# Performance work log

Hardware: AMD Instinct MI355X
Metric: run time of the kernel (lower is better)

Reference implementation:

```python
import jax, jax.numpy as jnp
import numpy as np

B, S, D = 2, 2048, 2048
H, KVH, DH = 16, 4, 128  # n_heads, n_kv_heads, head_dim
N_REP = H // KVH
THETA = 10000.0


def setup_inputs() -> dict:
    key = jax.random.key(0)
    ks = jax.random.split(key, 6)
    x = jax.random.normal(ks[0], (B, S, D), dtype=jnp.float32)
    wq = jax.random.normal(ks[1], (H * DH, D), dtype=jnp.float32) * (D ** -0.5)
    wk = jax.random.normal(ks[2], (KVH * DH, D), dtype=jnp.float32) * (D ** -0.5)
    wv = jax.random.normal(ks[3], (KVH * DH, D), dtype=jnp.float32) * (D ** -0.5)
    wo = jax.random.normal(ks[4], (D, H * DH), dtype=jnp.float32) * (D ** -0.5)
    # RoPE frequencies (complex freqs -> cos/sin), shape [S, DH//2]
    inv_freq = 1.0 / (THETA ** (np.arange(0, DH, 2, dtype=np.float32) / DH))
    angles = np.arange(S, dtype=np.float32)[:, None] * inv_freq[None, :]
    freqs_cos = jnp.asarray(np.cos(angles))
    freqs_sin = jnp.asarray(np.sin(angles))
    # causal additive mask [1,1,S,S]
    neg = jnp.full((S, S), -1e9, dtype=jnp.float32)
    mask = jnp.triu(neg, k=1)[None, None]
    return {"x": x, "freqs_cos": freqs_cos, "freqs_sin": freqs_sin,
            "mask": mask, "wq": wq, "wk": wk, "wv": wv, "wo": wo}


def _rope(t, cos, sin):
    # t: [B,S,h,DH]; cos/sin: [S,DH//2] -> broadcast [1,S,1,DH//2]
    tp = t.reshape(*t.shape[:-1], -1, 2)
    tr, ti = tp[..., 0], tp[..., 1]
    c = cos[None, :, None, :]
    s = sin[None, :, None, :]
    out_r = tr * c - ti * s
    out_i = tr * s + ti * c
    return jnp.stack([out_r, out_i], axis=-1).reshape(t.shape)


def reference(x, freqs_cos, freqs_sin, mask, wq, wk, wv, wo):
    b, s, _ = x.shape
    xq = jnp.einsum('bsd,ed->bse', x, wq).reshape(b, s, H, DH)
    xk = jnp.einsum('bsd,ed->bse', x, wk).reshape(b, s, KVH, DH)
    xv = jnp.einsum('bsd,ed->bse', x, wv).reshape(b, s, KVH, DH)
    xq = _rope(xq, freqs_cos, freqs_sin)
    xk = _rope(xk, freqs_cos, freqs_sin)
    # GQA: repeat kv heads
    xk = jnp.repeat(xk, N_REP, axis=2)
    xv = jnp.repeat(xv, N_REP, axis=2)
    q = xq.transpose(0, 2, 1, 3)  # [B,H,S,DH]
    k = xk.transpose(0, 2, 1, 3)
    v = xv.transpose(0, 2, 1, 3)
    scores = jnp.einsum('bhqd,bhkd->bhqk', q, k) / jnp.sqrt(jnp.float32(DH))
    scores = scores + mask
    attn = jax.nn.softmax(scores.astype(jnp.float32), axis=-1).astype(q.dtype)
    out = jnp.einsum('bhqk,bhkd->bhqd', attn, v)
    out = out.transpose(0, 2, 1, 3).reshape(b, s, H * DH)
    return jnp.einsum('bse,de->bsd', out, wo)
```

## Files before the change

kernel.cpp:

```cpp
#include <hip/hip_runtime.h>

#define Bq   2
#define Sq   2048
#define Dq   2048
#define Hq   16
#define KVHq 4
#define DHq  128

typedef unsigned short u16;
typedef short  bf16x8 __attribute__((ext_vector_type(8)));
typedef float  f32x4  __attribute__((ext_vector_type(4)));
typedef float  f32x16 __attribute__((ext_vector_type(16)));
typedef unsigned short u16x2 __attribute__((ext_vector_type(2)));
typedef unsigned short u16x4 __attribute__((ext_vector_type(4)));
typedef unsigned uu32x4 __attribute__((ext_vector_type(4)));

__device__ __forceinline__ u16 f2bf(float f) {
    unsigned u = __float_as_uint(f);
    u += 0x7fffu + ((u >> 16) & 1u);
    return (u16)(u >> 16);
}
__device__ __forceinline__ float bf2f(u16 s) {
    return __uint_as_float(((unsigned)s) << 16);
}

__device__ __forceinline__ unsigned cvtpk(float a, float b) {
    unsigned r;
    asm("v_cvt_pk_bf16_f32 %0, %1, %2" : "=v"(r) : "v"(a), "v"(b));
    return r;
}
__device__ __forceinline__ void pl32swap(unsigned& a, unsigned& b) {
    asm("v_permlane32_swap_b32 %0, %1" : "+v"(a), "+v"(b));
}
__device__ __forceinline__ bf16x8 mkfrag(unsigned w0, unsigned w1, unsigned w2, unsigned w3) {
    uu32x4 t = {w0, w1, w2, w3};
    return __builtin_bit_cast(bf16x8, t);
}

__global__ void cast_bf16(const float* __restrict__ in, u16* __restrict__ out, int n4) {
    int i = blockIdx.x * 256 + threadIdx.x;
    if (i >= n4) return;
    float4 v = ((const float4*)in)[i];
    u16x4 o;
    o.x = f2bf(v.x); o.y = f2bf(v.y); o.z = f2bf(v.z); o.w = f2bf(v.w);
    ((u16x4*)out)[i] = o;
}

__global__ void cast_weights(const float* __restrict__ wq, const float* __restrict__ wk,
                             const float* __restrict__ wv, const float* __restrict__ wo,
                             u16* __restrict__ wqb, u16* __restrict__ wkvb,
                             u16* __restrict__ wob) {
    int i = blockIdx.x * 256 + threadIdx.x;
    const float4* src; u16x4* dst; int off;
    if (i < 1048576)      { src = (const float4*)wq; dst = (u16x4*)wqb;  off = i; }
    else if (i < 1310720) { src = (const float4*)wk; dst = (u16x4*)wkvb; off = i - 1048576; }
    else if (i < 1572864) { src = (const float4*)wv; dst = (u16x4*)wkvb + 262144; off = i - 1310720; }
    else                  { src = (const float4*)wo; dst = (u16x4*)wob;  off = i - 1572864; }
    float4 v = src[off];
    u16x4 o;
    o.x = f2bf(v.x); o.y = f2bf(v.y); o.z = f2bf(v.z); o.w = f2bf(v.w);
    dst[off] = o;
}

__device__ __forceinline__ void async16(const void* g, void* l) {
    __builtin_amdgcn_global_load_lds(
        (const __attribute__((address_space(1))) unsigned*)g,
        (__attribute__((address_space(3))) unsigned*)l, 16, 0, 0);
}

__device__ __forceinline__ void stc(u16* p, float v)   { *p = f2bf(v); }
__device__ __forceinline__ void stc(float* p, float v) { *p = v; }

template <typename OutT>
__global__ __launch_bounds__(256) void gemm_nt(
    const u16* __restrict__ A, const u16* __restrict__ W, OutT* __restrict__ C,
    int M, int N, int K)
{
    __shared__ __align__(16) u16 lA[128 * 32];
    __shared__ __align__(16) u16 lB[128 * 32];

    const int t    = threadIdx.x;
    const int w    = t >> 6;
    const int lane = t & 63;
    const int lr   = lane & 15;
    const int quad = lane >> 4;
    const int wm   = (w >> 1) * 64, wn = (w & 1) * 64;
    const int bm   = blockIdx.x * 128, bn = blockIdx.y * 128;

    const u16* Ab = A + (size_t)bm * K;
    const u16* Wb = W + (size_t)bn * K;

    const int r0  = t >> 2;
    const int r1  = (256 + t) >> 2;
    const int kc0 = (t & 3) * 8;

    char* la0 = (char*)lA + w * 1024;
    char* la1 = (char*)lA + 4096 + w * 1024;
    char* lb0 = (char*)lB + w * 1024;
    char* lb1 = (char*)lB + 4096 + w * 1024;

    f32x4 acc[4][4] = {};

    for (int kt = 0; kt < K; kt += 32) {
        async16(Ab + (size_t)r0 * K + kt + kc0, la0);
        async16(Ab + (size_t)r1 * K + kt + kc0, la1);
        async16(Wb + (size_t)r0 * K + kt + kc0, lb0);
        async16(Wb + (size_t)r1 * K + kt + kc0, lb1);
        __syncthreads();

        bf16x8 af[4], bfr[4];
#pragma unroll
        for (int i = 0; i < 4; i++)
            af[i] = *(const bf16x8*)&lA[(wm + i * 16 + lr) * 32 + quad * 8];
#pragma unroll
        for (int j = 0; j < 4; j++)
            bfr[j] = *(const bf16x8*)&lB[(wn + j * 16 + lr) * 32 + quad * 8];
#pragma unroll
        for (int i = 0; i < 4; i++)
#pragma unroll
            for (int j = 0; j < 4; j++)
                acc[i][j] = __builtin_amdgcn_mfma_f32_16x16x32_bf16(af[i], bfr[j], acc[i][j], 0, 0, 0);
        __syncthreads();
    }

#pragma unroll
    for (int i = 0; i < 4; i++)
#pragma unroll
        for (int j = 0; j < 4; j++)
#pragma unroll
            for (int r = 0; r < 4; r++) {
                int gm = bm + wm + i * 16 + quad * 4 + r;
                int gn = bn + wn + j * 16 + lr;
                stc(C + (size_t)gm * N + gn, acc[i][j][r]);
            }
}

__global__ void rope_k(u16* __restrict__ T, const float* __restrict__ Cs,
                       const float* __restrict__ Sn, int lognh, int total) {
    int i = blockIdx.x * 256 + threadIdx.x;
    if (i >= total) return;
    int p  = i & 63;
    int sh = i >> 6;
    int s  = (sh >> lognh) & (Sq - 1);
    float c = Cs[s * 64 + p], sn = Sn[s * 64 + p];
    u16x2* ptr = ((u16x2*)T) + i;
    u16x2 v = *ptr;
    float tr = bf2f(v.x), ti = bf2f(v.y);
    u16x2 ov;
    ov.x = f2bf(tr * c - ti * sn);
    ov.y = f2bf(tr * sn + ti * c);
    *ptr = ov;
}

__global__ void rope_kv(u16* __restrict__ KV, const float* __restrict__ Cs,
                        const float* __restrict__ Sn, int total) {
    int i = blockIdx.x * 256 + threadIdx.x;
    if (i >= total) return;
    int p     = i & 63;
    int kvh   = (i >> 6) & 3;
    int token = i >> 8;
    int s     = token & (Sq - 1);
    float c = Cs[s * 64 + p], sn = Sn[s * 64 + p];
    u16x2* ptr = ((u16x2*)KV) + (size_t)token * 512 + kvh * 64 + p;
    u16x2 v = *ptr;
    float tr = bf2f(v.x), ti = bf2f(v.y);
    u16x2 ov;
    ov.x = f2bf(tr * c - ti * sn);
    ov.y = f2bf(tr * sn + ti * c);
    *ptr = ov;
}

__global__ void transpose_v_k(const u16* __restrict__ KV, u16* __restrict__ Vt) {
    __shared__ u16 tile[32][33];
    const int bk = blockIdx.z;
    const int b = bk >> 2, kvh = bk & 3;
    const int s0 = blockIdx.x * 32, d0 = blockIdx.y * 32;
    const int tx = threadIdx.x, ty = threadIdx.y;
    tile[ty][tx] = KV[(size_t)(b * Sq + s0 + ty) * 1024 + 512 + kvh * 128 + d0 + tx];
    __syncthreads();
    Vt[((size_t)bk * DHq + d0 + ty) * Sq + s0 + tx] = tile[tx][ty];
}

#define PSCALE 0.12753102f
#define PBIAS  17.31234049f

__global__ __launch_bounds__(256, 2) void flash_attn_sk2(
    const u16* __restrict__ Q, const u16* __restrict__ KV,
    const u16* __restrict__ Vt, float* __restrict__ Oc, float* __restrict__ Lc)
{
    __shared__ __align__(16) u16 kl[2][4 * 64 * 32];
    __shared__ __align__(16) u16 vl[2][2 * 128 * 32];

    const int bh = blockIdx.x;
    const int b = bh >> 4, h = bh & 15;
    const int kvh = h >> 2;
    const int c = 39 - (int)blockIdx.y;
    int qt, ci, nc;
    if (c < 4)       { qt = c;                    ci = 0;            nc = 1; }
    else if (c < 12) { qt = 4  + ((c - 4) >> 1);  ci = (c - 4) & 1;  nc = 2; }
    else if (c < 24) { qt = 8  + (c - 12) / 3;    ci = (c - 12) % 3; nc = 3; }
    else             { qt = 12 + ((c - 24) >> 2); ci = (c - 24) & 3; nc = 4; }
    const int T  = 2 * (qt + 1);
    const int t0 = (ci * T) / nc, t1 = ((ci + 1) * T) / nc;

    const int tid = threadIdx.x;
    const int w = tid >> 6, lane = tid & 63;
    const int col = lane & 31, hi = lane >> 5;
    const int q0 = qt * 128 + w * 32;
    const int qg = q0 + col;

    const u16* Qp = Q + (size_t)(b * Sq + qg) * (Hq * DHq) + h * DHq + hi * 8;
    bf16x8 qf[8];
#pragma unroll
    for (int ks = 0; ks < 8; ks++) qf[ks] = *(const bf16x8*)(Qp + ks * 16);

    const u16* Kg = KV + (size_t)b * Sq * 1024 + kvh * DHq;
    const u16* Vg = Vt + (size_t)(b * KVHq + kvh) * DHq * Sq;

    const int srow = lane >> 2;
    const int swl  = ((lane & 3) ^ ((lane >> 3) & 3)) * 8;
    const int xsw  = (col >> 1) & 3;

    f32x16 o[4] = {};
    float lsum = 0.f;

    auto STAGE = [&](int kt, int bsel) {
        const int kb = kt * 64;
#pragma unroll
        for (int c4 = 0; c4 < 4; c4++) {
            const u16* g = Kg + (size_t)(kb + w * 16 + srow) * 1024 + c4 * 32 + swl;
            async16(g, (char*)kl[bsel] + (c4 * 2048 + w * 512) * 2 + lane * 16);
        }
#pragma unroll
        for (int c4 = 0; c4 < 4; c4++) {
            const int g2 = c4 & 1, dbase = (c4 >> 1) * 64;
            const u16* g = Vg + (size_t)(dbase + w * 16 + srow) * Sq + kb + g2 * 32 + swl;
            async16(g, (char*)vl[bsel] + (g2 * 4096 + (dbase + w * 16) * 32) * 2 + lane * 16);
        }
    };

    STAGE(t0, 0);
    __syncthreads();

    int cur = 0;
    for (int kt = t0; kt < t1; kt++) {
        if (kt + 1 < t1) STAGE(kt + 1, cur ^ 1);

        const int kb = kt * 64;
        const u16* klc = kl[cur];
        const u16* vlc = vl[cur];

        f32x16 s0 = {}, s1 = {};
        __builtin_amdgcn_s_setprio(1);
#pragma unroll
        for (int ks = 0; ks < 8; ks++) {
            const int ch     = (((ks & 1) * 2 + hi) ^ xsw) * 8;
            const int kkbase = (ks >> 1) * 2048 + ch;
            bf16x8 k0 = *(const bf16x8*)&klc[kkbase + col * 32];
            bf16x8 k1 = *(const bf16x8*)&klc[kkbase + (32 + col) * 32];
            s0 = __builtin_amdgcn_mfma_f32_32x32x16_bf16(k0, qf[ks], s0, 0, 0, 0);
            s1 = __builtin_amdgcn_mfma_f32_32x32x16_bf16(k1, qf[ks], s1, 0, 0, 0);
        }
        __builtin_amdgcn_s_setprio(0);

        float p0a[16], p1a[16];
        float ls = 0.f;
        if (q0 - kb >= 63) {
#pragma unroll
            for (int r = 0; r < 16; r++) {
                float a0 = exp2f(s0[r] * PSCALE - PBIAS);
                float a1 = exp2f(s1[r] * PSCALE - PBIAS);
                ls += a0 + a1;
                p0a[r] = a0; p1a[r] = a1;
            }
        } else {
            const int thr = qg - kb;
#pragma unroll
            for (int r = 0; r < 16; r++) {
                const int kloc = (r & 3) + 8 * (r >> 2) + 4 * hi;
                float a0 = (kloc <= thr)      ? exp2f(s0[r] * PSCALE - PBIAS) : 0.f;
                float a1 = (kloc + 32 <= thr) ? exp2f(s1[r] * PSCALE - PBIAS) : 0.f;
                ls += a0 + a1;
                p0a[r] = a0; p1a[r] = a1;
            }
        }
        lsum += ls;

        __builtin_amdgcn_s_setprio(1);
#define PV_HALF(PARR, KSBASE)                                                      \
        {                                                                          \
            _Pragma("unroll")                                                      \
            for (int k2 = 0; k2 < 2; k2++) {                                       \
                const int bb = k2 * 8;                                             \
                unsigned wa = cvtpk(PARR[bb + 0], PARR[bb + 1]);                   \
                unsigned wb = cvtpk(PARR[bb + 4], PARR[bb + 5]);                   \
                pl32swap(wa, wb);                                                  \
                unsigned wc = cvtpk(PARR[bb + 2], PARR[bb + 3]);                   \
                unsigned wd = cvtpk(PARR[bb + 6], PARR[bb + 7]);                   \
                pl32swap(wc, wd);                                                  \
                bf16x8 pa = mkfrag(wa, wc, wb, wd);                                \
                const int vch   = ((k2 * 2 + hi) ^ xsw) * 8;                       \
                const int vbase = (((KSBASE) >> 1) * 4096) + vch;                  \
                _Pragma("unroll")                                                  \
                for (int n = 0; n < 4; n++) {                                      \
                    bf16x8 vf = *(const bf16x8*)&vlc[vbase + (n * 32 + col) * 32]; \
                    o[n] = __builtin_amdgcn_mfma_f32_32x32x16_bf16(pa, vf, o[n], 0, 0, 0); \
                }                                                                  \
            }                                                                      \
        }
        PV_HALF(p0a, 0)
        PV_HALF(p1a, 2)
#undef PV_HALF
        __builtin_amdgcn_s_setprio(0);

        if (kt + 1 < t1) __syncthreads();
        cur ^= 1;
    }

    float tot = lsum + __shfl_xor(lsum, 32);
    float* Ocb = Oc + (size_t)(bh * 40 + c) * 16384 + (size_t)w * 32 * 128;
    float* Lcb = Lc + (size_t)(bh * 40 + c) * 128 + w * 32;
    if (hi == 0) Lcb[col] = tot;
#pragma unroll
    for (int r = 0; r < 16; r++) {
        const int rloc = (r & 3) + 8 * (r >> 2) + 4 * hi;
#pragma unroll
        for (int n = 0; n < 4; n++)
            Ocb[rloc * 128 + n * 32 + col] = o[n][r];
    }
}

__global__ __launch_bounds__(256) void flash_reduce2(
    const float* __restrict__ Oc, const float* __restrict__ Lc, u16* __restrict__ AO)
{
    const int bh = blockIdx.x;
    const int qt = blockIdx.y;
    const int e  = blockIdx.z * 256 + threadIdx.x;
    const int row = e >> 5, col4 = e & 31;
    int cst, nc;
    if (qt < 4)       { cst = qt;                 nc = 1; }
    else if (qt < 8)  { cst = 4  + 2 * (qt - 4);  nc = 2; }
    else if (qt < 12) { cst = 12 + 3 * (qt - 8);  nc = 3; }
    else              { cst = 24 + 4 * (qt - 12); nc = 4; }
    f32x4 acc = {0.f, 0.f, 0.f, 0.f};
    float l = 0.f;
    for (int i = 0; i < nc; i++) {
        const size_t base = (size_t)(bh * 40 + cst + i);
        acc += ((const f32x4*)(Oc + base * 16384))[e];
        l   += Lc[base * 128 + row];
    }
    const float inv = 1.0f / l;
    const int b = bh >> 4, h = bh & 15;
    u16x4 ov;
    ov.x = f2bf(acc[0] * inv); ov.y = f2bf(acc[1] * inv);
    ov.z = f2bf(acc[2] * inv); ov.w = f2bf(acc[3] * inv);
    u16* dst = AO + (size_t)(b * Sq + qt * 128 + row) * (Hq * DHq) + h * DHq + col4 * 4;
    *(u16x4*)dst = ov;
}

__global__ __launch_bounds__(256) void flash_attn(
    const u16* __restrict__ Q, const u16* __restrict__ KV,
    const u16* __restrict__ Vt, u16* __restrict__ O)
{
    __shared__ __align__(16) u16 plds[4][16 * 72];
    const int bh = blockIdx.x;
    const int b = bh >> 4, h = bh & 15;
    const int kvh = h >> 2;
    const int w = threadIdx.x >> 6, lane = threadIdx.x & 63;
    const int lr = lane & 15, quad = lane >> 4;
    const int yy = gridDim.y - 1 - blockIdx.y;
    const int q0 = yy * 64 + w * 16;

    const u16* Qp = Q + (size_t)(b * Sq + q0 + lr) * (Hq * DHq) + h * DHq + quad * 8;
    bf16x8 qf[4];
#pragma unroll
    for (int kk = 0; kk < 4; kk++) qf[kk] = *(const bf16x8*)(Qp + kk * 32);

    const u16* Kp = KV + (size_t)b * Sq * 1024 + kvh * DHq;
    const u16* Vp = Vt + (size_t)(b * KVHq + kvh) * DHq * Sq;

    f32x4 o[8] = {};
    float lsum[4] = {0.f, 0.f, 0.f, 0.f};

    const int nt = (q0 + 16 + 63) >> 6;
    for (int kt = 0; kt < nt; kt++) {
        const int kb = kt * 64;
        f32x4 s[4] = {};
#pragma unroll
        for (int kk = 0; kk < 4; kk++) {
#pragma unroll
            for (int j = 0; j < 4; j++) {
                bf16x8 kf = *(const bf16x8*)(Kp + (size_t)(kb + j * 16 + lr) * 1024 + kk * 32 + quad * 8);
                s[j] = __builtin_amdgcn_mfma_f32_16x16x32_bf16(qf[kk], kf, s[j], 0, 0, 0);
            }
        }
#pragma unroll
        for (int r = 0; r < 4; r++) {
            const int qg = q0 + quad * 4 + r;
#pragma unroll
            for (int j = 0; j < 4; j++) {
                float v = s[j][r] * PSCALE - PBIAS;
                float p = (kb + j * 16 + lr <= qg) ? exp2f(v) : 0.f;
                lsum[r] += p;
                plds[w][(quad * 4 + r) * 72 + j * 16 + lr] = f2bf(p);
            }
        }
        bf16x8 pa0 = *(const bf16x8*)&plds[w][lr * 72 + quad * 8];
        bf16x8 pa1 = *(const bf16x8*)&plds[w][lr * 72 + 32 + quad * 8];
#pragma unroll
        for (int dt = 0; dt < 8; dt++) {
            bf16x8 v0 = *(const bf16x8*)(Vp + (size_t)(dt * 16 + lr) * Sq + kb + quad * 8);
            bf16x8 v1 = *(const bf16x8*)(Vp + (size_t)(dt * 16 + lr) * Sq + kb + 32 + quad * 8);
            o[dt] = __builtin_amdgcn_mfma_f32_16x16x32_bf16(pa0, v0, o[dt], 0, 0, 0);
            o[dt] = __builtin_amdgcn_mfma_f32_16x16x32_bf16(pa1, v1, o[dt], 0, 0, 0);
        }
    }

    u16* Ob = O + (size_t)(b * Sq) * (Hq * DHq) + h * DHq;
#pragma unroll
    for (int r = 0; r < 4; r++) {
        float t = lsum[r];
        t += __shfl_xor(t, 1);
        t += __shfl_xor(t, 2);
        t += __shfl_xor(t, 4);
        t += __shfl_xor(t, 8);
        const float inv = 1.0f / t;
        const int qg = q0 + quad * 4 + r;
#pragma unroll
        for (int dt = 0; dt < 8; dt++)
            Ob[(size_t)qg * (Hq * DHq) + dt * 16 + lr] = f2bf(o[dt][r] * inv);
    }
}

extern "C" void kernel_launch(void* const* d_in, const int* in_sizes, int n_in,
                              void* d_out, int out_size, void* d_ws, size_t ws_size,
                              hipStream_t stream) {
    const float* x  = (const float*)d_in[0];
    const float* fc = (const float*)d_in[1];
    const float* fs = (const float*)d_in[2];
    const float* wq = (const float*)d_in[4];
    const float* wk = (const float*)d_in[5];
    const float* wv = (const float*)d_in[6];
    const float* wo = (const float*)d_in[7];
    float* out = (float*)d_out;

    char* ws = (char*)d_ws;
    u16* xb   = (u16*)(ws);
    u16* wqb  = (u16*)(ws + 16777216);
    u16* wkvb = (u16*)(ws + 25165824);
    u16* wob  = (u16*)(ws + 29360128);
    u16* Qb   = (u16*)(ws + 37748736);
    u16* KVb  = (u16*)(ws + 54525952);
    u16* Vtb  = (u16*)(ws + 62914560);
    u16* AOb  = (u16*)(ws + 67108864);
    float* Ocb = (float*)(ws + 83886080);
    float* Lcb = (float*)(ws + 167772160);
    const size_t WS_NEED = 168427520;

    cast_bf16<<<8192, 256, 0, stream>>>(x, xb, 2097152);
    cast_weights<<<10240, 256, 0, stream>>>(wq, wk, wv, wo, wqb, wkvb, wob);

    dim3 blk(256);
    gemm_nt<u16><<<dim3(32, 16), blk, 0, stream>>>(xb, wqb,  Qb,  4096, 2048, 2048);
    gemm_nt<u16><<<dim3(32, 8),  blk, 0, stream>>>(xb, wkvb, KVb, 4096, 1024, 2048);

    rope_k<<<16384, 256, 0, stream>>>(Qb, fc, fs, 4, 4194304);
    rope_kv<<<4096, 256, 0, stream>>>(KVb, fc, fs, 1048576);

    transpose_v_k<<<dim3(64, 4, 8), dim3(32, 32), 0, stream>>>(KVb, Vtb);

    if (ws_size >= WS_NEED) {
        flash_attn_sk2<<<dim3(32, 40), blk, 0, stream>>>(Qb, KVb, Vtb, Ocb, Lcb);
        flash_reduce2<<<dim3(32, 16, 16), blk, 0, stream>>>(Ocb, Lcb, AOb);
    } else {
        flash_attn<<<dim3(32, 32), blk, 0, stream>>>(Qb, KVb, Vtb, AOb);
    }

    gemm_nt<float><<<dim3(32, 16), blk, 0, stream>>>(AOb, wob, out, 4096, 2048, 2048);
}
```

Before: 381.4 us.

## Fuse QKV projections with RoPE epilogue and merge cast kernels

Replaces the separate Q and KV GEMMs with one GEMM over the contiguous Q/K/V weight block, and applies RoPE in its epilogue. The epilogue uses a lane xor-shuffle to fetch each value's rotary partner, and writes Q or KV outputs by column range. This removes two standalone RoPE read-modify-write passes over Q and KV, plus extra kernel launches. The input and weight cast kernels are merged into one launch. The epilogue now loads cos/sin per element and branches per block, which adds some scalar work to the GEMM tail.

```diff
diff --git a/kernel.cpp b/kernel.cpp
--- a/kernel.cpp
+++ b/kernel.cpp
@@ -37,25 +37,21 @@
     return __builtin_bit_cast(bf16x8, t);
 }
 
-__global__ void cast_bf16(const float* __restrict__ in, u16* __restrict__ out, int n4) {
-    int i = blockIdx.x * 256 + threadIdx.x;
-    if (i >= n4) return;
-    float4 v = ((const float4*)in)[i];
-    u16x4 o;
-    o.x = f2bf(v.x); o.y = f2bf(v.y); o.z = f2bf(v.z); o.w = f2bf(v.w);
-    ((u16x4*)out)[i] = o;
-}
-
-__global__ void cast_weights(const float* __restrict__ wq, const float* __restrict__ wk,
-                             const float* __restrict__ wv, const float* __restrict__ wo,
-                             u16* __restrict__ wqb, u16* __restrict__ wkvb,
-                             u16* __restrict__ wob) {
+__global__ void cast_all(const float* __restrict__ x,
+                         const float* __restrict__ wq, const float* __restrict__ wk,
+                         const float* __restrict__ wv, const float* __restrict__ wo,
+                         u16* __restrict__ xb, u16* __restrict__ wqb,
+                         u16* __restrict__ wkvb, u16* __restrict__ wob) {
     int i = blockIdx.x * 256 + threadIdx.x;
     const float4* src; u16x4* dst; int off;
-    if (i < 1048576)      { src = (const float4*)wq; dst = (u16x4*)wqb;  off = i; }
-    else if (i < 1310720) { src = (const float4*)wk; dst = (u16x4*)wkvb; off = i - 1048576; }
-    else if (i < 1572864) { src = (const float4*)wv; dst = (u16x4*)wkvb + 262144; off = i - 1310720; }
-    else                  { src = (const float4*)wo; dst = (u16x4*)wob;  off = i - 1572864; }
+    if (i < 2097152) { src = (const float4*)x; dst = (u16x4*)xb; off = i; }
+    else {
+        int j = i - 2097152;
+        if (j < 1048576)      { src = (const float4*)wq; dst = (u16x4*)wqb;  off = j; }
+        else if (j < 1310720) { src = (const float4*)wk; dst = (u16x4*)wkvb; off = j - 1048576; }
+        else if (j < 1572864) { src = (const float4*)wv; dst = (u16x4*)wkvb + 262144; off = j - 1310720; }
+        else                  { src = (const float4*)wo; dst = (u16x4*)wob;  off = j - 1572864; }
+    }
     float4 v = src[off];
     u16x4 o;
     o.x = f2bf(v.x); o.y = f2bf(v.y); o.z = f2bf(v.z); o.w = f2bf(v.w);
@@ -135,39 +131,81 @@
             }
 }
 
-__global__ void rope_k(u16* __restrict__ T, const float* __restrict__ Cs,
-                       const float* __restrict__ Sn, int lognh, int total) {
-    int i = blockIdx.x * 256 + threadIdx.x;
-    if (i >= total) return;
-    int p  = i & 63;
-    int sh = i >> 6;
-    int s  = (sh >> lognh) & (Sq - 1);
-    float c = Cs[s * 64 + p], sn = Sn[s * 64 + p];
-    u16x2* ptr = ((u16x2*)T) + i;
-    u16x2 v = *ptr;
-    float tr = bf2f(v.x), ti = bf2f(v.y);
-    u16x2 ov;
-    ov.x = f2bf(tr * c - ti * sn);
-    ov.y = f2bf(tr * sn + ti * c);
-    *ptr = ov;
-}
-
-__global__ void rope_kv(u16* __restrict__ KV, const float* __restrict__ Cs,
-                        const float* __restrict__ Sn, int total) {
-    int i = blockIdx.x * 256 + threadIdx.x;
-    if (i >= total) return;
-    int p     = i & 63;
-    int kvh   = (i >> 6) & 3;
-    int token = i >> 8;
-    int s     = token & (Sq - 1);
-    float c = Cs[s * 64 + p], sn = Sn[s * 64 + p];
-    u16x2* ptr = ((u16x2*)KV) + (size_t)token * 512 + kvh * 64 + p;
-    u16x2 v = *ptr;
-    float tr = bf2f(v.x), ti = bf2f(v.y);
-    u16x2 ov;
-    ov.x = f2bf(tr * c - ti * sn);
-    ov.y = f2bf(tr * sn + ti * c);
-    *ptr = ov;
+__global__ __launch_bounds__(256) void gemm_qkv(
+    const u16* __restrict__ A, const u16* __restrict__ W,
+    u16* __restrict__ Qo, u16* __restrict__ KVo,
+    const float* __restrict__ Cs, const float* __restrict__ Sn)
+{
+    __shared__ __align__(16) u16 lA[128 * 32];
+    __shared__ __align__(16) u16 lB[128 * 32];
+    const int K = 2048;
+
+    const int t    = threadIdx.x;
+    const int w    = t >> 6;
+    const int lane = t & 63;
+    const int lr   = lane & 15;
+    const int quad = lane >> 4;
+    const int wm   = (w >> 1) * 64, wn = (w & 1) * 64;
+    const int bm   = blockIdx.x * 128, bn = blockIdx.y * 128;
+
+    const u16* Ab = A + (size_t)bm * K;
+    const u16* Wb = W + (size_t)bn * K;
+
+    const int r0  = t >> 2;
+    const int r1  = (256 + t) >> 2;
+    const int kc0 = (t & 3) * 8;
+
+    char* la0 = (char*)lA + w * 1024;
+    char* la1 = (char*)lA + 4096 + w * 1024;
+    char* lb0 = (char*)lB + w * 1024;
+    char* lb1 = (char*)lB + 4096 + w * 1024;
+
+    f32x4 acc[4][4] = {};
+
+    for (int kt = 0; kt < K; kt += 32) {
+        async16(Ab + (size_t)r0 * K + kt + kc0, la0);
+        async16(Ab + (size_t)r1 * K + kt + kc0, la1);
+        async16(Wb + (size_t)r0 * K + kt + kc0, lb0);
+        async16(Wb + (size_t)r1 * K + kt + kc0, lb1);
+        __syncthreads();
+
+        bf16x8 af[4], bfr[4];
+#pragma unroll
+        for (int i = 0; i < 4; i++)
+            af[i] = *(const bf16x8*)&lA[(wm + i * 16 + lr) * 32 + quad * 8];
+#pragma unroll
+        for (int j = 0; j < 4; j++)
+            bfr[j] = *(const bf16x8*)&lB[(wn + j * 16 + lr) * 32 + quad * 8];
+#pragma unroll
+        for (int i = 0; i < 4; i++)
+#pragma unroll
+            for (int j = 0; j < 4; j++)
+                acc[i][j] = __builtin_amdgcn_mfma_f32_16x16x32_bf16(af[i], bfr[j], acc[i][j], 0, 0, 0);
+        __syncthreads();
+    }
+
+    const bool doRope = (bn < 2560);
+    const bool isQ    = (bn < 2048);
+#pragma unroll
+    for (int i = 0; i < 4; i++)
+#pragma unroll
+        for (int j = 0; j < 4; j++)
+#pragma unroll
+            for (int r = 0; r < 4; r++) {
+                const int gm = bm + wm + i * 16 + quad * 4 + r;
+                const int gn = bn + wn + j * 16 + lr;
+                float v  = acc[i][j][r];
+                float pv = __shfl_xor(v, 1);
+                if (doRope) {
+                    const int s = gm & (Sq - 1);
+                    const int p = (gn & 127) >> 1;
+                    const float cc = Cs[s * 64 + p], ss = Sn[s * 64 + p];
+                    v = (gn & 1) ? (pv * ss + v * cc) : (v * cc - pv * ss);
+                }
+                const u16 ov = f2bf(v);
+                if (isQ) Qo [(size_t)gm * 2048 + gn]          = ov;
+                else     KVo[(size_t)gm * 1024 + (gn - 2048)] = ov;
+            }
 }
 
 __global__ void transpose_v_k(const u16* __restrict__ KV, u16* __restrict__ Vt) {
@@ -457,15 +495,10 @@
     float* Lcb = (float*)(ws + 167772160);
     const size_t WS_NEED = 168427520;
 
-    cast_bf16<<<8192, 256, 0, stream>>>(x, xb, 2097152);
-    cast_weights<<<10240, 256, 0, stream>>>(wq, wk, wv, wo, wqb, wkvb, wob);
+    cast_all<<<18432, 256, 0, stream>>>(x, wq, wk, wv, wo, xb, wqb, wkvb, wob);
 
     dim3 blk(256);
-    gemm_nt<u16><<<dim3(32, 16), blk, 0, stream>>>(xb, wqb,  Qb,  4096, 2048, 2048);
-    gemm_nt<u16><<<dim3(32, 8),  blk, 0, stream>>>(xb, wkvb, KVb, 4096, 1024, 2048);
-
-    rope_k<<<16384, 256, 0, stream>>>(Qb, fc, fs, 4, 4194304);
-    rope_kv<<<4096, 256, 0, stream>>>(KVb, fc, fs, 1048576);
+    gemm_qkv<<<dim3(32, 24), blk, 0, stream>>>(xb, wqb, Qb, KVb, fc, fs);
 
     transpose_v_k<<<dim3(64, 4, 8), dim3(32, 32), 0, stream>>>(KVb, Vtb);
 
```

Result: no change. 382.6 us (+0.3%).
